# Kernel optimization log

Hardware: AMD Instinct MI355X
Metric: run time of the kernel (lower is better)

The kernel has to match this reference:

```python
import jax, jax.numpy as jnp
import numpy as np
import math

D_K = 1024
HEADS = 16
HEAD_DIM = 64

def setup_inputs() -> dict:
    key = jax.random.key(0)
    ks = jax.random.split(key, 9)
    B, S, E = 2, 2048, D_K
    sc = 0.02
    return {
        "x": jax.random.normal(ks[0], (B, S, E), dtype=jnp.float32),
        "mask": 1,
        "Wq": jax.random.normal(ks[1], (E, E), dtype=jnp.float32) * sc,
        "bq": jnp.zeros((E,), dtype=jnp.float32),
        "Wk": jax.random.normal(ks[2], (E, E), dtype=jnp.float32) * sc,
        "bk": jnp.zeros((E,), dtype=jnp.float32),
        "Wv": jax.random.normal(ks[3], (E, E), dtype=jnp.float32) * sc,
        "bv": jnp.zeros((E,), dtype=jnp.float32),
        "Wo": jax.random.normal(ks[4], (E, E), dtype=jnp.float32) * sc,
        "bo": jnp.zeros((E,), dtype=jnp.float32),
    }

def reference(x, mask, Wq, bq, Wk, bk, Wv, bv, Wo, bo):
    B, S, E = x.shape
    H, Dh = HEADS, HEAD_DIM
    # QKV projections; split heads: [B, H, S, Dh]
    q = (x @ Wq + bq).reshape(B, S, H, Dh).transpose(0, 2, 1, 3)
    k = (x @ Wk + bk).reshape(B, S, H, Dh).transpose(0, 2, 1, 3)
    v = (x @ Wv + bv).reshape(B, S, H, Dh).transpose(0, 2, 1, 3)
    # NOTE: original scales by sqrt(d_k) (full model dim), not sqrt(head_dim)
    scores = jnp.einsum('bhsd,bhtd->bhst', q, k) / math.sqrt(E)
    if mask:
        causal = jnp.tril(jnp.ones((S, S), dtype=bool))
        scores = jnp.where(causal[None, None], scores, jnp.float32(-1e9))
    attn = jax.nn.softmax(scores, axis=-1)
    out = jnp.einsum('bhst,bhtd->bhsd', attn, v)  # [B,H,S,Dh]
    out = out.transpose(0, 2, 1, 3).reshape(B, S, E)
    return out @ Wo + bo
```

## Files before the change

kernel.cpp:

```cpp
#include <hip/hip_runtime.h>

#define HEADS  16
#define DH     64
#define SEQ    2048
#define NBATCH 2
#define EMB    1024
#define MTOT   (NBATCH * SEQ)

#define QSCALE 0.045084220027780106f

typedef short  s16x8 __attribute__((ext_vector_type(8)));
typedef float  f32x4 __attribute__((ext_vector_type(4)));
typedef unsigned short u16;
typedef unsigned short u16x4 __attribute__((ext_vector_type(4)));

__device__ __forceinline__ u16 f2bf(float f) {
  unsigned u = __builtin_bit_cast(unsigned, f);
  u += 0x7fffu + ((u >> 16) & 1u);
  return (u16)(u >> 16);
}

__device__ __forceinline__ void gll16(const u16* g, u16* l) {
  __builtin_amdgcn_global_load_lds(
      (const __attribute__((address_space(1))) unsigned int*)g,
      (__attribute__((address_space(3))) unsigned int*)l, 16, 0, 0);
}

__global__ void cvt_fused(const float* __restrict__ x, u16* __restrict__ xb,
                          const float* __restrict__ Wq, const float* __restrict__ Wk,
                          const float* __restrict__ Wv, const float* __restrict__ Wo,
                          u16* __restrict__ Wqt, u16* __restrict__ Wkt,
                          u16* __restrict__ Wvt, u16* __restrict__ Wot) {
  int tx = threadIdx.x, ty = threadIdx.y;
  if (blockIdx.z == 4) {
    int tid = ty * 32 + tx;
    int base = (blockIdx.y * 32 + blockIdx.x) * 4096;
#pragma unroll
    for (int j = 0; j < 4; j++) {
      int i = base + j * 1024 + tid * 4;
      float4 v = *(const float4*)(x + i);
      u16x4 o;
      o.x = f2bf(v.x); o.y = f2bf(v.y); o.z = f2bf(v.z); o.w = f2bf(v.w);
      *(u16x4*)(xb + i) = o;
    }
    return;
  }
  __shared__ float tile[32][33];
  const float* W; u16* T;
  switch (blockIdx.z) {
    case 0:  W = Wq; T = Wqt; break;
    case 1:  W = Wk; T = Wkt; break;
    case 2:  W = Wv; T = Wvt; break;
    default: W = Wo; T = Wot; break;
  }
  int n0 = blockIdx.x * 32, k0 = blockIdx.y * 32;
#pragma unroll
  for (int r = 0; r < 32; r += 8)
    tile[ty + r][tx] = W[(size_t)(k0 + ty + r) * EMB + n0 + tx];
  __syncthreads();
#pragma unroll
  for (int r = 0; r < 32; r += 8)
    T[(size_t)(n0 + ty + r) * EMB + k0 + tx] = f2bf(tile[tx][ty + r]);
}

__device__ __forceinline__ void gemm_core(const u16* __restrict__ A, const u16* __restrict__ Bt,
                                          u16* As, u16* Bs, int m0, int n0, f32x4 acc[4][2]) {
  const int tid = threadIdx.x;
  const int lane = tid & 63, w = tid >> 6;
  const int wm = w >> 1, wn = w & 1;
  const int lr = lane & 15, lq = lane >> 4;
#pragma unroll
  for (int i = 0; i < 4; i++)
#pragma unroll
    for (int j = 0; j < 2; j++)
      acc[i][j] = (f32x4){0.f, 0.f, 0.f, 0.f};

  for (int k0 = 0; k0 < EMB; k0 += 64) {
    __syncthreads();
#pragma unroll
    for (int j = 0; j < 4; j++) {
      int c = tid + 256 * j;
      int row = c >> 3, c8 = (c & 7) ^ (row & 7);
      gll16(&A[(size_t)(m0 + row) * EMB + k0 + c8 * 8],
            &As[(w * 64 + 256 * j) * 8]);
    }
#pragma unroll
    for (int j = 0; j < 2; j++) {
      int c = tid + 256 * j;
      int row = c >> 3, c8 = (c & 7) ^ (row & 7);
      gll16(&Bt[(size_t)(n0 + row) * EMB + k0 + c8 * 8],
            &Bs[(w * 64 + 256 * j) * 8]);
    }
    __syncthreads();
#pragma unroll
    for (int kk8 = 0; kk8 < 8; kk8 += 4) {
      s16x8 af[4], bf[2];
#pragma unroll
      for (int i = 0; i < 4; i++) {
        int row = wm * 64 + i * 16 + lr;
        af[i] = *(const s16x8*)&As[row * 64 + (((kk8 + lq) ^ (row & 7)) * 8)];
      }
#pragma unroll
      for (int j = 0; j < 2; j++) {
        int row = wn * 32 + j * 16 + lr;
        bf[j] = *(const s16x8*)&Bs[row * 64 + (((kk8 + lq) ^ (row & 7)) * 8)];
      }
#pragma unroll
      for (int i = 0; i < 4; i++)
#pragma unroll
        for (int j = 0; j < 2; j++)
          acc[i][j] = __builtin_amdgcn_mfma_f32_16x16x32_bf16(af[i], bf[j], acc[i][j], 0, 0, 0);
    }
  }
}

__global__ __launch_bounds__(256) void gemm_qkv(const u16* __restrict__ xb,
                                                const u16* __restrict__ Wqt, const u16* __restrict__ Wkt,
                                                const u16* __restrict__ Wvt,
                                                const float* __restrict__ bq, const float* __restrict__ bk,
                                                const float* __restrict__ bv,
                                                u16* __restrict__ Qb, u16* __restrict__ Kb,
                                                u16* __restrict__ Vtb) {
  __shared__ __align__(16) u16 As[128 * 64];
  __shared__ __align__(16) u16 Bs[64 * 64];
  const int lin  = blockIdx.x + 16 * (blockIdx.y + 32 * blockIdx.z);
  const int job  = (lin & 7) * 192 + (lin >> 3);
  const int mode = job >> 9;
  const int rem  = job & 511;
  const int m0 = (rem >> 4) * 128, n0 = (rem & 15) * 64;

  const u16* Bt; const float* bias; u16* out;
  switch (mode) {
    case 0:  Bt = Wqt; bias = bq; out = Qb;  break;
    case 1:  Bt = Wkt; bias = bk; out = Kb;  break;
    default: Bt = Wvt; bias = bv; out = Vtb; break;
  }
  f32x4 acc[4][2];
  gemm_core(xb, Bt, As, Bs, m0, n0, acc);

  const int tid = threadIdx.x, lane = tid & 63, w = tid >> 6;
  const int wm = w >> 1, wn = w & 1;
  const int lr = lane & 15, lq = lane >> 4;
#pragma unroll
  for (int i = 0; i < 4; i++) {
#pragma unroll
    for (int j = 0; j < 2; j++) {
      int col   = n0 + wn * 32 + j * 16 + lr;
      int mbase = m0 + wm * 64 + i * 16 + lq * 4;
      float bv_ = bias[col];
      int h = col >> 6, d = col & 63;
      if (mode == 0) {
#pragma unroll
        for (int r = 0; r < 4; r++) {
          int m = mbase + r, b = m >> 11, s = m & (SEQ - 1);
          out[((size_t)(b * HEADS + h) * SEQ + s) * DH + d] = f2bf((acc[i][j][r] + bv_) * QSCALE);
        }
      } else if (mode == 1) {
#pragma unroll
        for (int r = 0; r < 4; r++) {
          int m = mbase + r, b = m >> 11, s = m & (SEQ - 1);
          out[((size_t)(b * HEADS + h) * SEQ + s) * DH + d] = f2bf(acc[i][j][r] + bv_);
        }
      } else {
        int b = mbase >> 11, s = mbase & (SEQ - 1);
        u16x4 pk;
        pk.x = f2bf(acc[i][j][0] + bv_);
        pk.y = f2bf(acc[i][j][1] + bv_);
        pk.z = f2bf(acc[i][j][2] + bv_);
        pk.w = f2bf(acc[i][j][3] + bv_);
        *(u16x4*)&out[((size_t)(b * HEADS + h) * DH + d) * SEQ + s] = pk;
      }
    }
  }
}

__global__ __launch_bounds__(256) void gemm_out(const u16* __restrict__ A, const u16* __restrict__ Bt,
                                                const float* __restrict__ bias, float* __restrict__ out) {
  __shared__ __align__(16) u16 As[128 * 64];
  __shared__ __align__(16) u16 Bs[64 * 64];
  const int lin = blockIdx.x + 16 * blockIdx.y;
  const int job = (lin & 7) * 64 + (lin >> 3);
  const int m0 = (job >> 4) * 128, n0 = (job & 15) * 64;
  f32x4 acc[4][2];
  gemm_core(A, Bt, As, Bs, m0, n0, acc);

  const int tid = threadIdx.x, lane = tid & 63, w = tid >> 6;
  const int wm = w >> 1, wn = w & 1;
  const int lr = lane & 15, lq = lane >> 4;
#pragma unroll
  for (int i = 0; i < 4; i++) {
#pragma unroll
    for (int j = 0; j < 2; j++) {
      int col   = n0 + wn * 32 + j * 16 + lr;
      int mbase = m0 + wm * 64 + i * 16 + lq * 4;
      float bv_ = bias[col];
#pragma unroll
      for (int r = 0; r < 4; r++)
        out[(size_t)(mbase + r) * EMB + col] = acc[i][j][r] + bv_;
    }
  }
}

__global__ __launch_bounds__(512, 4) void attn_fwd(const u16* __restrict__ Q,
                                                   const u16* __restrict__ Kg,
                                                   const u16* __restrict__ Vt,
                                                   u16* __restrict__ O) {
  __shared__ __align__(16) u16 smem[33280];
  const int tid = threadIdx.x, lane = tid & 63, w = tid >> 6;
  const int g = w >> 2, wg = w & 3;
  const int lr = lane & 15, lq = lane >> 4;
  const int lin = blockIdx.x + 16 * blockIdx.y;
  const int job = (lin & 7) * 64 + (lin >> 3);
  const int bx = job & 15, bh = job >> 4;
  const int qtA = bx, qtB = 31 - bx;
  const int rowoff = wg * 16;
  u16* Ks = smem + (g ? 11520 : 0);
  u16* Vs = smem + (g ? 16640 : 5120);
  u16* pw = smem + 23040 + w * 1280;
  const size_t qkbase = (size_t)bh * SEQ * DH;
  const size_t vbase  = (size_t)bh * DH * SEQ;
  const u16* kgp = Kg + qkbase;
  const u16* vtp = Vt + vbase;
  const int t256 = tid & 255;
  const int b = bh >> 4, hh = bh & 15;

  s16x8 qf0, qf1;
  {
    const int myqt0 = g ? qtB : qtA;
    const u16* qp = Q + qkbase + (size_t)(myqt0 * 64 + rowoff + lr) * DH;
    qf0 = *(const s16x8*)&qp[lq * 8];
    qf1 = *(const s16x8*)&qp[32 + lq * 8];
  }
  f32x4 o[4];
  float psum = 0.f;
#pragma unroll
  for (int t = 0; t < 4; t++) o[t] = (f32x4){0.f, 0.f, 0.f, 0.f};

  const int srow = t256 >> 3, soff = (t256 & 7) * 8;
  int kt0 = g ? (16 - bx) : 0;
  s16x8 kr0 = *(const s16x8*)&kgp[(size_t)(kt0 * 64 + srow) * DH + soff];
  s16x8 kr1 = *(const s16x8*)&kgp[(size_t)(kt0 * 64 + srow + 32) * DH + soff];
  s16x8 vr0 = *(const s16x8*)&vtp[(size_t)srow * SEQ + kt0 * 64 + soff];
  s16x8 vr1 = *(const s16x8*)&vtp[(size_t)(srow + 32) * SEQ + kt0 * 64 + soff];

  for (int i = 0; i < 17; ++i) {
    __syncthreads();
    *(s16x8*)&Ks[srow * 80 + soff]        = kr0;
    *(s16x8*)&Ks[(srow + 32) * 80 + soff] = kr1;
    *(s16x8*)&Vs[srow * 80 + soff]        = vr0;
    *(s16x8*)&Vs[(srow + 32) * 80 + soff] = vr1;
    __syncthreads();

    {
      bool hn = g ? (i + 1 < 16) : (i + 1 < 17);
      if (hn) {
        int ktn = g ? (17 + i - bx) : ((i + 1 <= qtA) ? (i + 1) : (i - qtA));
        kr0 = *(const s16x8*)&kgp[(size_t)(ktn * 64 + srow) * DH + soff];
        kr1 = *(const s16x8*)&kgp[(size_t)(ktn * 64 + srow + 32) * DH + soff];
        vr0 = *(const s16x8*)&vtp[(size_t)srow * SEQ + ktn * 64 + soff];
        vr1 = *(const s16x8*)&vtp[(size_t)(srow + 32) * SEQ + ktn * 64 + soff];
      }
    }

    if (g == 0 && i == qtA + 1) {
      float s2 = psum + __shfl_xor(psum, 16);
      float s4 = s2 + __shfl_xor(s2, 32);
      float inv[4];
#pragma unroll
      for (int r = 0; r < 4; r++)
        inv[r] = __builtin_amdgcn_rcpf(__shfl(s4, lq * 4 + r));
#pragma unroll
      for (int t = 0; t < 4; t++)
#pragma unroll
        for (int r = 0; r < 4; r++) {
          int m = b * SEQ + qtA * 64 + rowoff + lq * 4 + r;
          O[(size_t)m * EMB + hh * 64 + t * 16 + lr] = f2bf(o[t][r] * inv[r]);
        }
#pragma unroll
      for (int t = 0; t < 4; t++) o[t] = (f32x4){0.f, 0.f, 0.f, 0.f};
      psum = 0.f;
      const u16* qp = Q + qkbase + (size_t)(qtB * 64 + rowoff + lr) * DH;
      qf0 = *(const s16x8*)&qp[lq * 8];
      qf1 = *(const s16x8*)&qp[32 + lq * 8];
    }

    const bool docomp = g ? (i < 16) : true;
    if (docomp) {
      f32x4 sc[4];
      __builtin_amdgcn_s_setprio(1);
#pragma unroll
      for (int t = 0; t < 4; t++) {
        s16x8 kf0 = *(const s16x8*)&Ks[(t * 16 + lr) * 80 + lq * 8];
        s16x8 kf1 = *(const s16x8*)&Ks[(t * 16 + lr) * 80 + 32 + lq * 8];
        f32x4 z = (f32x4){0.f, 0.f, 0.f, 0.f};
        z = __builtin_amdgcn_mfma_f32_16x16x32_bf16(kf0, qf0, z, 0, 0, 0);
        z = __builtin_amdgcn_mfma_f32_16x16x32_bf16(kf1, qf1, z, 0, 0, 0);
        sc[t] = z;
      }
      __builtin_amdgcn_s_setprio(0);
      const bool diag = g ? (i == 15) : (i == qtA);
      if (diag) {
#pragma unroll
        for (int t = 0; t < 4; t++)
#pragma unroll
          for (int r = 0; r < 4; r++)
            if ((t * 16 + lq * 4 + r) > (rowoff + lr)) sc[t][r] = -1e9f;
      }

#pragma unroll
      for (int t = 0; t < 4; t++) {
        u16x4 pk;
#pragma unroll
        for (int r = 0; r < 4; r++) {
          float p = __builtin_amdgcn_exp2f(sc[t][r]);
          psum += p;
          pk[r] = f2bf(p);
        }
        *(u16x4*)&pw[lr * 80 + t * 16 + lq * 4] = pk;
      }

      __builtin_amdgcn_s_setprio(1);
#pragma unroll
      for (int kc = 0; kc < 2; kc++) {
        s16x8 pf = *(const s16x8*)&pw[lr * 80 + kc * 32 + lq * 8];
#pragma unroll
        for (int t = 0; t < 4; t++) {
          s16x8 vf = *(const s16x8*)&Vs[(t * 16 + lr) * 80 + kc * 32 + lq * 8];
          o[t] = __builtin_amdgcn_mfma_f32_16x16x32_bf16(pf, vf, o[t], 0, 0, 0);
        }
      }
      __builtin_amdgcn_s_setprio(0);
    }
  }

  __syncthreads();
  float* Cb = (float*)smem;
  float* Ss = (float*)(smem + 23040);
  if (g == 0) {
    float s2 = psum + __shfl_xor(psum, 16);
    float s4 = s2 + __shfl_xor(s2, 32);
    if (lq == 0) Ss[rowoff + lr] = s4;
#pragma unroll
    for (int t = 0; t < 4; t++)
#pragma unroll
      for (int r = 0; r < 4; r++)
        Cb[(rowoff + lq * 4 + r) * 68 + t * 16 + lr] = o[t][r];
  }
  __syncthreads();
  if (g == 1) {
    float s2 = psum + __shfl_xor(psum, 16);
    float s4 = s2 + __shfl_xor(s2, 32);
    float inv[4];
#pragma unroll
    for (int r = 0; r < 4; r++)
      inv[r] = __builtin_amdgcn_rcpf(__shfl(s4, lq * 4 + r) + Ss[rowoff + lq * 4 + r]);
#pragma unroll
    for (int t = 0; t < 4; t++)
#pragma unroll
      for (int r = 0; r < 4; r++) {
        int m = b * SEQ + qtB * 64 + rowoff + lq * 4 + r;
        float v = o[t][r] + Cb[(rowoff + lq * 4 + r) * 68 + t * 16 + lr];
        O[(size_t)m * EMB + hh * 64 + t * 16 + lr] = f2bf(v * inv[r]);
      }
  }
}

extern "C" void kernel_launch(void* const* d_in, const int* in_sizes, int n_in,
                              void* d_out, int out_size, void* d_ws, size_t ws_size,
                              hipStream_t stream) {
  const float* x  = (const float*)d_in[0];
  const float* Wq = (const float*)d_in[2];
  const float* bq = (const float*)d_in[3];
  const float* Wk = (const float*)d_in[4];
  const float* bk = (const float*)d_in[5];
  const float* Wv = (const float*)d_in[6];
  const float* bv = (const float*)d_in[7];
  const float* Wo = (const float*)d_in[8];
  const float* bo = (const float*)d_in[9];

  char* ws = (char*)d_ws;
  const size_t MB = 1024 * 1024;
  u16* Qb  = (u16*)(ws + 0 * MB);
  u16* Kb  = (u16*)(ws + 8 * MB);
  u16* Vtb = (u16*)(ws + 16 * MB);
  u16* xb  = (u16*)(ws + 24 * MB);
  u16* Ob  = xb;
  u16* Wqt = (u16*)(ws + 32 * MB);
  u16* Wkt = (u16*)(ws + 34 * MB);
  u16* Wvt = (u16*)(ws + 36 * MB);
  u16* Wot = (u16*)(ws + 38 * MB);

  cvt_fused<<<dim3(32, 32, 5), dim3(32, 8), 0, stream>>>(
      x, xb, Wq, Wk, Wv, Wo, Wqt, Wkt, Wvt, Wot);

  gemm_qkv<<<dim3(EMB / 64, MTOT / 128, 3), 256, 0, stream>>>(
      xb, Wqt, Wkt, Wvt, bq, bk, bv, Qb, Kb, Vtb);

  attn_fwd<<<dim3(16, NBATCH * HEADS), 512, 0, stream>>>(Qb, Kb, Vtb, Ob);

  gemm_out<<<dim3(EMB / 64, MTOT / 128), 256, 0, stream>>>(Ob, Wot, bo, (float*)d_out);
}
```

Measured before the change: 175.5 us.

## Enlarge attention query tile to 128 rows with two 16-row blocks per wave

```diff
diff --git a/kernel.cpp b/kernel.cpp
--- a/kernel.cpp
+++ b/kernel.cpp
@@ -201,22 +201,23 @@
   }
 }
 
-__global__ __launch_bounds__(512, 4) void attn_fwd(const u16* __restrict__ Q,
+__global__ __launch_bounds__(512, 2) void attn_fwd(const u16* __restrict__ Q,
                                                    const u16* __restrict__ Kg,
                                                    const u16* __restrict__ Vt,
                                                    u16* __restrict__ O) {
-  __shared__ __align__(16) u16 smem[33280];
+  __shared__ __align__(16) u16 smem[40960];
   const int tid = threadIdx.x, lane = tid & 63, w = tid >> 6;
   const int g = w >> 2, wg = w & 3;
   const int lr = lane & 15, lq = lane >> 4;
-  const int lin = blockIdx.x + 16 * blockIdx.y;
-  const int job = (lin & 7) * 64 + (lin >> 3);
-  const int bx = job & 15, bh = job >> 4;
-  const int qtA = bx, qtB = 31 - bx;
-  const int rowoff = wg * 16;
-  u16* Ks = smem + (g ? 11520 : 0);
-  u16* Vs = smem + (g ? 16640 : 5120);
-  u16* pw = smem + 23040 + w * 1280;
+  const int lin = blockIdx.x + 8 * blockIdx.y;
+  const int job = (lin & 7) * 32 + (lin >> 3);
+  const int px = job & 7, bh = job >> 3;
+  const int pB = 15 - px;
+  const int qoff = wg * 32;
+  const int trans = 2 * px + 2;
+  u16* Ks = smem + (g ? 10240 : 0);
+  u16* Vs = smem + (g ? 15360 : 5120);
+  u16* pw = smem + 20480 + w * 2560;
   const size_t qkbase = (size_t)bh * SEQ * DH;
   const size_t vbase  = (size_t)bh * DH * SEQ;
   const u16* kgp = Kg + qkbase;
@@ -224,20 +225,24 @@
   const int t256 = tid & 255;
   const int b = bh >> 4, hh = bh & 15;
 
-  s16x8 qf0, qf1;
+  s16x8 qf[2][2];
+  int qbase = (g ? pB : px) * 128;
   {
-    const int myqt0 = g ? qtB : qtA;
-    const u16* qp = Q + qkbase + (size_t)(myqt0 * 64 + rowoff + lr) * DH;
-    qf0 = *(const s16x8*)&qp[lq * 8];
-    qf1 = *(const s16x8*)&qp[32 + lq * 8];
-  }
-  f32x4 o[4];
-  float psum = 0.f;
-#pragma unroll
-  for (int t = 0; t < 4; t++) o[t] = (f32x4){0.f, 0.f, 0.f, 0.f};
+    const u16* qp = Q + qkbase + (size_t)(qbase + qoff + lr) * DH;
+    qf[0][0] = *(const s16x8*)&qp[lq * 8];
+    qf[0][1] = *(const s16x8*)&qp[32 + lq * 8];
+    qf[1][0] = *(const s16x8*)&qp[16 * DH + lq * 8];
+    qf[1][1] = *(const s16x8*)&qp[16 * DH + 32 + lq * 8];
+  }
+  f32x4 o[2][4];
+  float psum[2] = {0.f, 0.f};
+#pragma unroll
+  for (int qb = 0; qb < 2; qb++)
+#pragma unroll
+    for (int t = 0; t < 4; t++) o[qb][t] = (f32x4){0.f, 0.f, 0.f, 0.f};
 
   const int srow = t256 >> 3, soff = (t256 & 7) * 8;
-  int kt0 = g ? (16 - bx) : 0;
+  int kt0 = g ? (15 - 2 * px) : 0;
   s16x8 kr0 = *(const s16x8*)&kgp[(size_t)(kt0 * 64 + srow) * DH + soff];
   s16x8 kr1 = *(const s16x8*)&kgp[(size_t)(kt0 * 64 + srow + 32) * DH + soff];
   s16x8 vr0 = *(const s16x8*)&vtp[(size_t)srow * SEQ + kt0 * 64 + soff];
@@ -251,117 +256,140 @@
     *(s16x8*)&Vs[(srow + 32) * 80 + soff] = vr1;
     __syncthreads();
 
-    {
-      bool hn = g ? (i + 1 < 16) : (i + 1 < 17);
-      if (hn) {
-        int ktn = g ? (17 + i - bx) : ((i + 1 <= qtA) ? (i + 1) : (i - qtA));
-        kr0 = *(const s16x8*)&kgp[(size_t)(ktn * 64 + srow) * DH + soff];
-        kr1 = *(const s16x8*)&kgp[(size_t)(ktn * 64 + srow + 32) * DH + soff];
-        vr0 = *(const s16x8*)&vtp[(size_t)srow * SEQ + ktn * 64 + soff];
-        vr1 = *(const s16x8*)&vtp[(size_t)(srow + 32) * SEQ + ktn * 64 + soff];
-      }
-    }
-
-    if (g == 0 && i == qtA + 1) {
-      float s2 = psum + __shfl_xor(psum, 16);
+    if (i + 1 < 17) {
+      int ktn = g ? (16 - 2 * px + i)
+                  : ((i + 1 < trans) ? (i + 1) : (i + 1 - trans));
+      kr0 = *(const s16x8*)&kgp[(size_t)(ktn * 64 + srow) * DH + soff];
+      kr1 = *(const s16x8*)&kgp[(size_t)(ktn * 64 + srow + 32) * DH + soff];
+      vr0 = *(const s16x8*)&vtp[(size_t)srow * SEQ + ktn * 64 + soff];
+      vr1 = *(const s16x8*)&vtp[(size_t)(srow + 32) * SEQ + ktn * 64 + soff];
+    }
+
+    if (g == 0 && i == trans) {
+#pragma unroll
+      for (int qb = 0; qb < 2; qb++) {
+        float s2 = psum[qb] + __shfl_xor(psum[qb], 16);
+        float s4 = s2 + __shfl_xor(s2, 32);
+        float inv[4];
+#pragma unroll
+        for (int r = 0; r < 4; r++) inv[r] = __builtin_amdgcn_rcpf(__shfl(s4, lq * 4 + r));
+#pragma unroll
+        for (int t = 0; t < 4; t++)
+#pragma unroll
+          for (int r = 0; r < 4; r++) {
+            int m = b * SEQ + px * 128 + qoff + qb * 16 + lq * 4 + r;
+            O[(size_t)m * EMB + hh * 64 + t * 16 + lr] = f2bf(o[qb][t][r] * inv[r]);
+          }
+#pragma unroll
+        for (int t = 0; t < 4; t++) o[qb][t] = (f32x4){0.f, 0.f, 0.f, 0.f};
+        psum[qb] = 0.f;
+      }
+      qbase = pB * 128;
+      const u16* qp = Q + qkbase + (size_t)(qbase + qoff + lr) * DH;
+      qf[0][0] = *(const s16x8*)&qp[lq * 8];
+      qf[0][1] = *(const s16x8*)&qp[32 + lq * 8];
+      qf[1][0] = *(const s16x8*)&qp[16 * DH + lq * 8];
+      qf[1][1] = *(const s16x8*)&qp[16 * DH + 32 + lq * 8];
+    }
+
+    const int j = g ? (15 - 2 * px + i) : ((i < trans) ? i : (i - trans));
+
+    f32x4 sc[2][4];
+    __builtin_amdgcn_s_setprio(1);
+#pragma unroll
+    for (int t = 0; t < 4; t++) {
+      s16x8 kf0 = *(const s16x8*)&Ks[(t * 16 + lr) * 80 + lq * 8];
+      s16x8 kf1 = *(const s16x8*)&Ks[(t * 16 + lr) * 80 + 32 + lq * 8];
+#pragma unroll
+      for (int qb = 0; qb < 2; qb++) {
+        f32x4 z = (f32x4){0.f, 0.f, 0.f, 0.f};
+        z = __builtin_amdgcn_mfma_f32_16x16x32_bf16(kf0, qf[qb][0], z, 0, 0, 0);
+        z = __builtin_amdgcn_mfma_f32_16x16x32_bf16(kf1, qf[qb][1], z, 0, 0, 0);
+        sc[qb][t] = z;
+      }
+    }
+    __builtin_amdgcn_s_setprio(0);
+
+#pragma unroll
+    for (int qb = 0; qb < 2; qb++) {
+      int qmin = qbase + qoff + qb * 16;
+      if (64 * j + 63 > qmin) {
+        int gq = qmin + lr;
+#pragma unroll
+        for (int t = 0; t < 4; t++)
+#pragma unroll
+          for (int r = 0; r < 4; r++)
+            if (64 * j + t * 16 + lq * 4 + r > gq) sc[qb][t][r] = -1e9f;
+      }
+    }
+
+#pragma unroll
+    for (int qb = 0; qb < 2; qb++)
+#pragma unroll
+      for (int t = 0; t < 4; t++) {
+        u16x4 pk;
+#pragma unroll
+        for (int r = 0; r < 4; r++) {
+          float p = __builtin_amdgcn_exp2f(sc[qb][t][r]);
+          psum[qb] += p;
+          pk[r] = f2bf(p);
+        }
+        *(u16x4*)&pw[(qb * 16 + lr) * 80 + t * 16 + lq * 4] = pk;
+      }
+
+    __builtin_amdgcn_s_setprio(1);
+#pragma unroll
+    for (int kc = 0; kc < 2; kc++) {
+      s16x8 pf[2];
+#pragma unroll
+      for (int qb = 0; qb < 2; qb++)
+        pf[qb] = *(const s16x8*)&pw[(qb * 16 + lr) * 80 + kc * 32 + lq * 8];
+#pragma unroll
+      for (int t = 0; t < 4; t++) {
+        s16x8 vf = *(const s16x8*)&Vs[(t * 16 + lr) * 80 + kc * 32 + lq * 8];
+#pragma unroll
+        for (int qb = 0; qb < 2; qb++)
+          o[qb][t] = __builtin_amdgcn_mfma_f32_16x16x32_bf16(pf[qb], vf, o[qb][t], 0, 0, 0);
+      }
+    }
+    __builtin_amdgcn_s_setprio(0);
+  }
+
+  __syncthreads();
+  float* Cb = (float*)smem;
+  float* Ss = (float*)(smem + 20480);
+  if (g == 0) {
+#pragma unroll
+    for (int qb = 0; qb < 2; qb++) {
+      float s2 = psum[qb] + __shfl_xor(psum[qb], 16);
+      float s4 = s2 + __shfl_xor(s2, 32);
+      if (lq == 0) Ss[qoff + qb * 16 + lr] = s4;
+#pragma unroll
+      for (int t = 0; t < 4; t++)
+#pragma unroll
+        for (int r = 0; r < 4; r++)
+          Cb[(qoff + qb * 16 + lq * 4 + r) * 68 + t * 16 + lr] = o[qb][t][r];
+    }
+  }
+  __syncthreads();
+  if (g == 1) {
+#pragma unroll
+    for (int qb = 0; qb < 2; qb++) {
+      float s2 = psum[qb] + __shfl_xor(psum[qb], 16);
       float s4 = s2 + __shfl_xor(s2, 32);
       float inv[4];
 #pragma unroll
       for (int r = 0; r < 4; r++)
-        inv[r] = __builtin_amdgcn_rcpf(__shfl(s4, lq * 4 + r));
+        inv[r] = __builtin_amdgcn_rcpf(__shfl(s4, lq * 4 + r) + Ss[qoff + qb * 16 + lq * 4 + r]);
 #pragma unroll
       for (int t = 0; t < 4; t++)
 #pragma unroll
         for (int r = 0; r < 4; r++) {
-          int m = b * SEQ + qtA * 64 + rowoff + lq * 4 + r;
-          O[(size_t)m * EMB + hh * 64 + t * 16 + lr] = f2bf(o[t][r] * inv[r]);
+          int m = b * SEQ + pB * 128 + qoff + qb * 16 + lq * 4 + r;
+          float v = o[qb][t][r] + Cb[(qoff + qb * 16 + lq * 4 + r) * 68 + t * 16 + lr];
+          O[(size_t)m * EMB + hh * 64 + t * 16 + lr] = f2bf(v * inv[r]);
         }
-#pragma unroll
-      for (int t = 0; t < 4; t++) o[t] = (f32x4){0.f, 0.f, 0.f, 0.f};
-      psum = 0.f;
-      const u16* qp = Q + qkbase + (size_t)(qtB * 64 + rowoff + lr) * DH;
-      qf0 = *(const s16x8*)&qp[lq * 8];
-      qf1 = *(const s16x8*)&qp[32 + lq * 8];
-    }
-
-    const bool docomp = g ? (i < 16) : true;
-    if (docomp) {
-      f32x4 sc[4];
-      __builtin_amdgcn_s_setprio(1);
-#pragma unroll
-      for (int t = 0; t < 4; t++) {
-        s16x8 kf0 = *(const s16x8*)&Ks[(t * 16 + lr) * 80 + lq * 8];
-        s16x8 kf1 = *(const s16x8*)&Ks[(t * 16 + lr) * 80 + 32 + lq * 8];
-        f32x4 z = (f32x4){0.f, 0.f, 0.f, 0.f};
-        z = __builtin_amdgcn_mfma_f32_16x16x32_bf16(kf0, qf0, z, 0, 0, 0);
-        z = __builtin_amdgcn_mfma_f32_16x16x32_bf16(kf1, qf1, z, 0, 0, 0);
-        sc[t] = z;
-      }
-      __builtin_amdgcn_s_setprio(0);
-      const bool diag = g ? (i == 15) : (i == qtA);
-      if (diag) {
-#pragma unroll
-        for (int t = 0; t < 4; t++)
-#pragma unroll
-          for (int r = 0; r < 4; r++)
-            if ((t * 16 + lq * 4 + r) > (rowoff + lr)) sc[t][r] = -1e9f;
-      }
-
-#pragma unroll
-      for (int t = 0; t < 4; t++) {
-        u16x4 pk;
-#pragma unroll
-        for (int r = 0; r < 4; r++) {
-          float p = __builtin_amdgcn_exp2f(sc[t][r]);
-          psum += p;
-          pk[r] = f2bf(p);
-        }
-        *(u16x4*)&pw[lr * 80 + t * 16 + lq * 4] = pk;
-      }
-
-      __builtin_amdgcn_s_setprio(1);
-#pragma unroll
-      for (int kc = 0; kc < 2; kc++) {
-        s16x8 pf = *(const s16x8*)&pw[lr * 80 + kc * 32 + lq * 8];
-#pragma unroll
-        for (int t = 0; t < 4; t++) {
-          s16x8 vf = *(const s16x8*)&Vs[(t * 16 + lr) * 80 + kc * 32 + lq * 8];
-          o[t] = __builtin_amdgcn_mfma_f32_16x16x32_bf16(pf, vf, o[t], 0, 0, 0);
-        }
-      }
-      __builtin_amdgcn_s_setprio(0);
-    }
-  }
-
-  __syncthreads();
-  float* Cb = (float*)smem;
-  float* Ss = (float*)(smem + 23040);
-  if (g == 0) {
-    float s2 = psum + __shfl_xor(psum, 16);
-    float s4 = s2 + __shfl_xor(s2, 32);
-    if (lq == 0) Ss[rowoff + lr] = s4;
-#pragma unroll
-    for (int t = 0; t < 4; t++)
-#pragma unroll
-      for (int r = 0; r < 4; r++)
-        Cb[(rowoff + lq * 4 + r) * 68 + t * 16 + lr] = o[t][r];
-  }
-  __syncthreads();
-  if (g == 1) {
-    float s2 = psum + __shfl_xor(psum, 16);
-    float s4 = s2 + __shfl_xor(s2, 32);
-    float inv[4];
-#pragma unroll
-    for (int r = 0; r < 4; r++)
-      inv[r] = __builtin_amdgcn_rcpf(__shfl(s4, lq * 4 + r) + Ss[rowoff + lq * 4 + r]);
-#pragma unroll
-    for (int t = 0; t < 4; t++)
-#pragma unroll
-      for (int r = 0; r < 4; r++) {
-        int m = b * SEQ + qtB * 64 + rowoff + lq * 4 + r;
-        float v = o[t][r] + Cb[(rowoff + lq * 4 + r) * 68 + t * 16 + lr];
-        O[(size_t)m * EMB + hh * 64 + t * 16 + lr] = f2bf(v * inv[r]);
-      }
+    }
   }
 }
 
@@ -396,7 +424,7 @@
   gemm_qkv<<<dim3(EMB / 64, MTOT / 128, 3), 256, 0, stream>>>(
       xb, Wqt, Wkt, Wvt, bq, bk, bv, Qb, Kb, Vtb);
 
-  attn_fwd<<<dim3(16, NBATCH * HEADS), 512, 0, stream>>>(Qb, Kb, Vtb, Ob);
+  attn_fwd<<<dim3(8, 32), 512, 0, stream>>>(Qb, Kb, Vtb, Ob);
 
   gemm_out<<<dim3(EMB / 64, MTOT / 128), 256, 0, stream>>>(Ob, Wot, bo, (float*)d_out);
 }
```

Result: no change. 177.6 us (+1.2%).
